# Performance work log

Measured on AMD Instinct MI355X. Metric: run time of the kernel, lower is better.

The kernel has to match this reference:

```python
import jax, jax.numpy as jnp
import numpy as np

N_NODES = 50000
N_EDGES = 800000
IN_CH, HIDDEN, OUT_CH = 64, 16, 8


def setup_inputs() -> dict:
    key = jax.random.key(0)
    ks = jax.random.split(key, 8)
    x = jax.random.normal(ks[0], (N_NODES, IN_CH), dtype=jnp.float32)
    edge_index = jax.random.randint(ks[1], (2, N_EDGES), 0, N_NODES, dtype=jnp.int64)
    # SAGEConv params: lin_l (neighbor aggregate, has bias), lin_r (root, no bias)
    s1 = 1.0 / np.sqrt(IN_CH)
    s2 = 1.0 / np.sqrt(HIDDEN)
    W1l = jax.random.uniform(ks[2], (HIDDEN, IN_CH), jnp.float32, -s1, s1)
    W1r = jax.random.uniform(ks[3], (HIDDEN, IN_CH), jnp.float32, -s1, s1)
    b1 = jax.random.uniform(ks[4], (HIDDEN,), jnp.float32, -s1, s1)
    W2l = jax.random.uniform(ks[5], (OUT_CH, HIDDEN), jnp.float32, -s2, s2)
    W2r = jax.random.uniform(ks[6], (OUT_CH, HIDDEN), jnp.float32, -s2, s2)
    b2 = jax.random.uniform(ks[7], (OUT_CH,), jnp.float32, -s2, s2)
    return {"x": x, "W1l": W1l, "W1r": W1r, "b1": b1,
            "W2l": W2l, "W2r": W2r, "b2": b2, "edge_index": edge_index}


def _sage_conv(x, src, dst, Wl, Wr, b, n_nodes):
    # mean-aggregate neighbor features: gather from src, scatter-mean to dst
    msg_sum = jax.ops.segment_sum(x[src], dst, num_segments=n_nodes)  # [N, d]
    deg = jax.ops.segment_sum(jnp.ones((src.shape[0], 1), x.dtype), dst,
                              num_segments=n_nodes)                    # [N, 1]
    aggr = msg_sum / jnp.maximum(deg, 1.0)
    # out = lin_l(aggr) + lin_r(x); bias lives in lin_l
    return aggr @ Wl.T + x @ Wr.T + b


def reference(x, W1l, W1r, b1, W2l, W2r, b2, edge_index):
    src, dst = edge_index[0], edge_index[1]
    n = x.shape[0]
    h = jax.nn.relu(_sage_conv(x, src, dst, W1l, W1r, b1, n))
    # F.dropout(p=0.1, training=self.training): identity in eval mode
    return _sage_conv(h, src, dst, W2l, W2r, b2, n)
```

## Files before the change

kernel.cpp:

```cpp
#include <hip/hip_runtime.h>

#define IN_CH 64
#define HID   16
#define OUTC  8
#define BINSHIFT 6
#define BINCAP  (1 << BINSHIFT)

#define CHUNK_A     1024
#define SLICE_SHIFT 8
#define SLICE_NODES 256
#define SUBCAP      24

typedef _Float16 half2_t __attribute__((ext_vector_type(2)));
typedef _Float16 half8_t __attribute__((ext_vector_type(8)));


__global__ __launch_bounds__(256) void build_xform(
    const float* __restrict__ x,
    const int*   __restrict__ esrc,
    const int*   __restrict__ edst,
    const float* __restrict__ W1l,
    const float* __restrict__ W1r,
    const float* __restrict__ b1,
    int* __restrict__ cnts,
    unsigned int* __restrict__ gbuf,
    _Float16* __restrict__ y1h,
    float* __restrict__ r1,
    int n_nodes, int n_edges, int nb_part)
{
    __shared__ __align__(16) float sWl[HID * 68];
    __shared__ __align__(16) float sWr[HID * 68];
    __shared__ __align__(16) float sx[16 * 68];
    __shared__ float sb1[HID];
    __shared__ int scurs[SLICE_NODES];

    int b   = blockIdx.x;
    int tid = threadIdx.x;

    if (b < nb_part) {
        int base = b * CHUNK_A;
        scurs[tid] = 0;
        __syncthreads();
#pragma unroll
        for (int j = 0; j < CHUNK_A / 256; ++j) {
            int e = base + j * 256 + tid;
            if (e < n_edges) {
                int d  = edst[e];
                int s  = esrc[e];
                int bk = d >> SLICE_SHIFT;
                int pos = atomicAdd(&scurs[bk], 1);
                if (pos < SUBCAP)
                    gbuf[((size_t)bk * nb_part + b) * SUBCAP + pos] =
                        (unsigned)(s & 0xFFFF) |
                        ((unsigned)(d & (SLICE_NODES - 1)) << 16);
            }
        }
        __syncthreads();
        int c = scurs[tid];
        cnts[(size_t)tid * nb_part + b] = c > SUBCAP ? SUBCAP : c;
        return;
    }

    for (int i = tid; i < HID * IN_CH; i += 256) {
        int c = i >> 6, k = i & 63;
        sWl[c * 68 + k] = W1l[i];
        sWr[c * 68 + k] = W1r[i];
    }
    if (tid < HID) sb1[tid] = b1[tid];

    int nl   = tid >> 4;
    int c    = tid & 15;
    int node = (b - nb_part) * 16 + nl;

    if (node < n_nodes)
        *(float4*)&sx[nl * 68 + c * 4] =
            *(const float4*)&x[(size_t)node * IN_CH + c * 4];
    __syncthreads();
    if (node >= n_nodes) return;

    float accL = 0.f, accR = 0.f;
#pragma unroll
    for (int k4 = 0; k4 < 16; ++k4) {
        float4 xv = *(const float4*)&sx [nl * 68 + k4 * 4];
        float4 wl = *(const float4*)&sWl[c  * 68 + k4 * 4];
        float4 wr = *(const float4*)&sWr[c  * 68 + k4 * 4];
        accL = fmaf(xv.x, wl.x, accL); accL = fmaf(xv.y, wl.y, accL);
        accL = fmaf(xv.z, wl.z, accL); accL = fmaf(xv.w, wl.w, accL);
        accR = fmaf(xv.x, wr.x, accR); accR = fmaf(xv.y, wr.y, accR);
        accR = fmaf(xv.z, wr.z, accR); accR = fmaf(xv.w, wr.w, accR);
    }
    y1h[(size_t)node * HID + c] = (_Float16)accL;
    r1 [(size_t)node * HID + c] = accR + sb1[c];
}

__global__ __launch_bounds__(256) void bin_build(
    const int* __restrict__ cnts,
    const unsigned int* __restrict__ gbuf,
    int* __restrict__ cur,
    unsigned short* __restrict__ adj,
    int n_nodes, int nb_part)
{
    __shared__ int scnt[SLICE_NODES];
    __shared__ __align__(16) unsigned short bins[SLICE_NODES * BINCAP];

    int b   = blockIdx.x;
    int tid = threadIdx.x;

    scnt[tid] = 0;
    __syncthreads();

    for (int a = tid; a < nb_part; a += 256) {
        int cnt = cnts[(size_t)b * nb_part + a];
        const unsigned int* bp = gbuf + ((size_t)b * nb_part + a) * SUBCAP;
        for (int i = 0; i < cnt; ++i) {
            unsigned p = bp[i];
            int dl  = p >> 16;
            int pos = atomicAdd(&scnt[dl], 1);
            if (pos < BINCAP)
                bins[(dl << BINSHIFT) + pos] = (unsigned short)(p & 0xFFFF);
        }
    }
    __syncthreads();

    int node0  = b << SLICE_SHIFT;
    int nvalid = n_nodes - node0;
    if (nvalid > SLICE_NODES) nvalid = SLICE_NODES;

    if (tid < nvalid) cur[node0 + tid] = scnt[tid];

    int nv = nvalid << 3;
    for (int i = tid; i < nv; i += 256)
        *(uint4*)(adj + ((size_t)node0 << BINSHIFT) + ((size_t)i << 3)) =
            *(const uint4*)&bins[(size_t)i << 3];
}

#define ACC8(v)                                                          \
    do {                                                                 \
        half2_t p01 = {(v).s0, (v).s1}, p23 = {(v).s2, (v).s3};          \
        half2_t p45 = {(v).s4, (v).s5}, p67 = {(v).s6, (v).s7};          \
        s0 = __builtin_amdgcn_fdot2(p01, k10, s0, false);                \
        s1 = __builtin_amdgcn_fdot2(p01, k01, s1, false);                \
        s2 = __builtin_amdgcn_fdot2(p23, k10, s2, false);                \
        s3 = __builtin_amdgcn_fdot2(p23, k01, s3, false);                \
        s4 = __builtin_amdgcn_fdot2(p45, k10, s4, false);                \
        s5 = __builtin_amdgcn_fdot2(p45, k01, s5, false);                \
        s6 = __builtin_amdgcn_fdot2(p67, k10, s6, false);                \
        s7 = __builtin_amdgcn_fdot2(p67, k01, s7, false);                \
    } while (0)

__global__ __launch_bounds__(256) void fused_gather(
    const float* __restrict__ r1,
    const _Float16* __restrict__ y1h,
    const int*   __restrict__ cur,
    const unsigned short* __restrict__ adj,
    const float* __restrict__ W2l, const float* __restrict__ W2r,
    const float* __restrict__ b2,
    _Float16* __restrict__ y2h, float* __restrict__ r2out,
    int n_nodes)
{
    __shared__ float sW2l[HID * OUTC];
    __shared__ float sW2r[HID * OUTC];
    __shared__ float sb2[OUTC];
    __shared__ float sh[32 * 17];

    int tid = threadIdx.x;
    for (int i = tid; i < HID * OUTC; i += 256) {
        int o = i >> 4, k = i & 15;
        sW2l[k * OUTC + o] = W2l[i];
        sW2r[k * OUTC + o] = W2r[i];
    }
    if (tid < OUTC) sb2[tid] = b2[tid];

    int nl   = tid >> 3;
    int t    = tid & 7;
    int h    = t >> 2;
    int ep   = t & 3;
    int node = blockIdx.x * 32 + nl;
    bool real = node < n_nodes;

    const half2_t k10 = {(_Float16)1.f, (_Float16)0.f};
    const half2_t k01 = {(_Float16)0.f, (_Float16)1.f};

    if (real) {
        int deg = cur[node];
        if (deg > BINCAP) deg = BINCAP;
        int iters = deg >> 2;
        float s0 = 0.f, s1 = 0.f, s2 = 0.f, s3 = 0.f;
        float s4 = 0.f, s5 = 0.f, s6 = 0.f, s7 = 0.f;
        const _Float16* yq = y1h + h * 8;
        const unsigned short* row = adj + ((size_t)node << BINSHIFT);
        const ushort4* ap = (const ushort4*)row;
        for (int it = ep; it < iters; it += 4) {
            ushort4 s = ap[it];
            half8_t v0 = *(const half8_t*)(yq + (size_t)s.x * HID);
            half8_t v1 = *(const half8_t*)(yq + (size_t)s.y * HID);
            half8_t v2 = *(const half8_t*)(yq + (size_t)s.z * HID);
            half8_t v3 = *(const half8_t*)(yq + (size_t)s.w * HID);
            ACC8(v0); ACC8(v1); ACC8(v2); ACC8(v3);
        }
        for (int g = (iters << 2) + ep; g < deg; g += 4) {
            half8_t v = *(const half8_t*)(yq + (size_t)row[g] * HID);
            ACC8(v);
        }
        s0 += __shfl_xor(s0, 1); s0 += __shfl_xor(s0, 2);
        s1 += __shfl_xor(s1, 1); s1 += __shfl_xor(s1, 2);
        s2 += __shfl_xor(s2, 1); s2 += __shfl_xor(s2, 2);
        s3 += __shfl_xor(s3, 1); s3 += __shfl_xor(s3, 2);
        s4 += __shfl_xor(s4, 1); s4 += __shfl_xor(s4, 2);
        s5 += __shfl_xor(s5, 1); s5 += __shfl_xor(s5, 2);
        s6 += __shfl_xor(s6, 1); s6 += __shfl_xor(s6, 2);
        s7 += __shfl_xor(s7, 1); s7 += __shfl_xor(s7, 2);

        if (ep == 0) {
            float inv = 1.0f / fmaxf((float)deg, 1.0f);
            const float* rr = &r1[(size_t)node * HID + h * 8];
            float4 ra = *(const float4*)(rr);
            float4 rb = *(const float4*)(rr + 4);
            float* shp = &sh[nl * 17 + h * 8];
            shp[0] = fmaxf(fmaf(s0, inv, ra.x), 0.f);
            shp[1] = fmaxf(fmaf(s1, inv, ra.y), 0.f);
            shp[2] = fmaxf(fmaf(s2, inv, ra.z), 0.f);
            shp[3] = fmaxf(fmaf(s3, inv, ra.w), 0.f);
            shp[4] = fmaxf(fmaf(s4, inv, rb.x), 0.f);
            shp[5] = fmaxf(fmaf(s5, inv, rb.y), 0.f);
            shp[6] = fmaxf(fmaf(s6, inv, rb.z), 0.f);
            shp[7] = fmaxf(fmaf(s7, inv, rb.w), 0.f);
        }
    }
    __syncthreads();
    if (!real) return;

    const float* hrow = &sh[nl * 17];
    float al = 0.f, ar = sb2[t];
#pragma unroll
    for (int k = 0; k < HID; ++k) {
        float hv = hrow[k];
        al = fmaf(hv, sW2l[k * OUTC + t], al);
        ar = fmaf(hv, sW2r[k * OUTC + t], ar);
    }
    y2h[(size_t)node * OUTC + t] = (_Float16)al;
    r2out[(size_t)node * OUTC + t] = ar;
}

__global__ __launch_bounds__(256) void gather_out(
    const _Float16* __restrict__ y2h,
    const int*   __restrict__ cur,
    const unsigned short* __restrict__ adj,
    float* __restrict__ out,
    int n_nodes)
{
    int tid  = threadIdx.x;
    int node = blockIdx.x * 64 + (tid >> 2);
    if (node >= n_nodes) return;
    int ep = tid & 3;

    int deg = cur[node];
    if (deg > BINCAP) deg = BINCAP;
    int iters = deg >> 2;
    const unsigned short* row = adj + ((size_t)node << BINSHIFT);
    const ushort4* ap = (const ushort4*)row;

    const half2_t k10 = {(_Float16)1.f, (_Float16)0.f};
    const half2_t k01 = {(_Float16)0.f, (_Float16)1.f};

    float s0 = 0.f, s1 = 0.f, s2 = 0.f, s3 = 0.f;
    float s4 = 0.f, s5 = 0.f, s6 = 0.f, s7 = 0.f;
    for (int it = ep; it < iters; it += 4) {
        ushort4 s = ap[it];
        half8_t v0 = *(const half8_t*)(y2h + (size_t)s.x * OUTC);
        half8_t v1 = *(const half8_t*)(y2h + (size_t)s.y * OUTC);
        half8_t v2 = *(const half8_t*)(y2h + (size_t)s.z * OUTC);
        half8_t v3 = *(const half8_t*)(y2h + (size_t)s.w * OUTC);
        ACC8(v0); ACC8(v1); ACC8(v2); ACC8(v3);
    }
    for (int g = (iters << 2) + ep; g < deg; g += 4) {
        half8_t v = *(const half8_t*)(y2h + (size_t)row[g] * OUTC);
        ACC8(v);
    }
    s0 += __shfl_xor(s0, 1); s0 += __shfl_xor(s0, 2);
    s1 += __shfl_xor(s1, 1); s1 += __shfl_xor(s1, 2);
    s2 += __shfl_xor(s2, 1); s2 += __shfl_xor(s2, 2);
    s3 += __shfl_xor(s3, 1); s3 += __shfl_xor(s3, 2);
    s4 += __shfl_xor(s4, 1); s4 += __shfl_xor(s4, 2);
    s5 += __shfl_xor(s5, 1); s5 += __shfl_xor(s5, 2);
    s6 += __shfl_xor(s6, 1); s6 += __shfl_xor(s6, 2);
    s7 += __shfl_xor(s7, 1); s7 += __shfl_xor(s7, 2);
    if (ep != 0) return;

    float inv = 1.0f / fmaxf((float)deg, 1.0f);
    float* op = out + (size_t)node * OUTC;
    float4 c0 = *(float4*)op;
    float4 c1 = *(float4*)(op + 4);
    c0.x = fmaf(s0, inv, c0.x); c0.y = fmaf(s1, inv, c0.y);
    c0.z = fmaf(s2, inv, c0.z); c0.w = fmaf(s3, inv, c0.w);
    c1.x = fmaf(s4, inv, c1.x); c1.y = fmaf(s5, inv, c1.y);
    c1.z = fmaf(s6, inv, c1.z); c1.w = fmaf(s7, inv, c1.w);
    *(float4*)op = c0;
    *(float4*)(op + 4) = c1;
}

extern "C" void kernel_launch(void* const* d_in, const int* in_sizes, int n_in,
                              void* d_out, int out_size, void* d_ws, size_t ws_size,
                              hipStream_t stream)
{
    const float* x   = (const float*)d_in[0];
    const float* W1l = (const float*)d_in[1];
    const float* W1r = (const float*)d_in[2];
    const float* b1  = (const float*)d_in[3];
    const float* W2l = (const float*)d_in[4];
    const float* W2r = (const float*)d_in[5];
    const float* b2  = (const float*)d_in[6];
    const int*   ei  = (const int*)d_in[7];

    int n_nodes = in_sizes[0] / IN_CH;
    int n_edges = in_sizes[7] / 2;
    const int* esrc = ei;
    const int* edst = ei + n_edges;

    float* out = (float*)d_out;

    dim3 blk(256);
    int nb_part = (n_edges + CHUNK_A - 1) / CHUNK_A;
    int nb_node = (n_nodes + 15) / 16;
    int ns      = (n_nodes + SLICE_NODES - 1) >> SLICE_SHIFT;

    char* wsb = (char*)d_ws;
    _Float16* y1h = (_Float16*)wsb;
    _Float16* y2h = y1h + (size_t)n_nodes * HID;
    float* r1 = (float*)(y2h + (size_t)n_nodes * OUTC);
    int* cur  = (int*)(r1 + (size_t)n_nodes * HID);
    unsigned short* adj = (unsigned short*)(cur + n_nodes);
    int* cnts = (int*)(adj + ((size_t)n_nodes << BINSHIFT));
    unsigned int* gbuf = (unsigned int*)(cnts + (size_t)SLICE_NODES * nb_part);

    build_xform<<<dim3(nb_part + nb_node), blk, 0, stream>>>(
        x, esrc, edst, W1l, W1r, b1, cnts, gbuf, y1h, r1,
        n_nodes, n_edges, nb_part);

    bin_build<<<dim3(ns), blk, 0, stream>>>(cnts, gbuf, cur, adj,
                                            n_nodes, nb_part);

    fused_gather<<<dim3((n_nodes + 31) / 32), blk, 0, stream>>>(
        r1, y1h, cur, adj, W2l, W2r, b2, y2h, out, n_nodes);

    gather_out<<<dim3((n_nodes + 63) / 64), blk, 0, stream>>>(
        y2h, cur, adj, out, n_nodes);
}
```

Measured before the change: 119.4 us.

## Merge four kernels into one cooperative persistent kernel with grid syncs

Replaces the four separate launches (edge partition plus layer-1 transform, bin build, fused layer-1 gather plus layer-2 transform, output gather) with a single cooperative kernel of fixed grid size that loops over virtual blocks and separates phases with grid.sync. The aim is to remove per-launch overhead and inter-kernel gaps. In exchange, the grid is capped at 1024 blocks with shared memory reused across phases, and each grid-wide barrier makes every block wait for the slowest one. The phase-2 split gives bin building a fixed set of blocks while the rest do the transform, so occupancy and load balance change.

```diff
diff --git a/kernel.cpp b/kernel.cpp
--- a/kernel.cpp
+++ b/kernel.cpp
@@ -1,4 +1,7 @@
 #include <hip/hip_runtime.h>
+#include <hip/hip_cooperative_groups.h>
+
+namespace cg = cooperative_groups;
 
 #define IN_CH 64
 #define HID   16
@@ -11,128 +14,12 @@
 #define SLICE_NODES 256
 #define SUBCAP      24
 
+#define NBLOCKS     1024
+#define SMEM_BYTES  33792
+
 typedef _Float16 half2_t __attribute__((ext_vector_type(2)));
 typedef _Float16 half8_t __attribute__((ext_vector_type(8)));
 
-
-__global__ __launch_bounds__(256) void build_xform(
-    const float* __restrict__ x,
-    const int*   __restrict__ esrc,
-    const int*   __restrict__ edst,
-    const float* __restrict__ W1l,
-    const float* __restrict__ W1r,
-    const float* __restrict__ b1,
-    int* __restrict__ cnts,
-    unsigned int* __restrict__ gbuf,
-    _Float16* __restrict__ y1h,
-    float* __restrict__ r1,
-    int n_nodes, int n_edges, int nb_part)
-{
-    __shared__ __align__(16) float sWl[HID * 68];
-    __shared__ __align__(16) float sWr[HID * 68];
-    __shared__ __align__(16) float sx[16 * 68];
-    __shared__ float sb1[HID];
-    __shared__ int scurs[SLICE_NODES];
-
-    int b   = blockIdx.x;
-    int tid = threadIdx.x;
-
-    if (b < nb_part) {
-        int base = b * CHUNK_A;
-        scurs[tid] = 0;
-        __syncthreads();
-#pragma unroll
-        for (int j = 0; j < CHUNK_A / 256; ++j) {
-            int e = base + j * 256 + tid;
-            if (e < n_edges) {
-                int d  = edst[e];
-                int s  = esrc[e];
-                int bk = d >> SLICE_SHIFT;
-                int pos = atomicAdd(&scurs[bk], 1);
-                if (pos < SUBCAP)
-                    gbuf[((size_t)bk * nb_part + b) * SUBCAP + pos] =
-                        (unsigned)(s & 0xFFFF) |
-                        ((unsigned)(d & (SLICE_NODES - 1)) << 16);
-            }
-        }
-        __syncthreads();
-        int c = scurs[tid];
-        cnts[(size_t)tid * nb_part + b] = c > SUBCAP ? SUBCAP : c;
-        return;
-    }
-
-    for (int i = tid; i < HID * IN_CH; i += 256) {
-        int c = i >> 6, k = i & 63;
-        sWl[c * 68 + k] = W1l[i];
-        sWr[c * 68 + k] = W1r[i];
-    }
-    if (tid < HID) sb1[tid] = b1[tid];
-
-    int nl   = tid >> 4;
-    int c    = tid & 15;
-    int node = (b - nb_part) * 16 + nl;
-
-    if (node < n_nodes)
-        *(float4*)&sx[nl * 68 + c * 4] =
-            *(const float4*)&x[(size_t)node * IN_CH + c * 4];
-    __syncthreads();
-    if (node >= n_nodes) return;
-
-    float accL = 0.f, accR = 0.f;
-#pragma unroll
-    for (int k4 = 0; k4 < 16; ++k4) {
-        float4 xv = *(const float4*)&sx [nl * 68 + k4 * 4];
-        float4 wl = *(const float4*)&sWl[c  * 68 + k4 * 4];
-        float4 wr = *(const float4*)&sWr[c  * 68 + k4 * 4];
-        accL = fmaf(xv.x, wl.x, accL); accL = fmaf(xv.y, wl.y, accL);
-        accL = fmaf(xv.z, wl.z, accL); accL = fmaf(xv.w, wl.w, accL);
-        accR = fmaf(xv.x, wr.x, accR); accR = fmaf(xv.y, wr.y, accR);
-        accR = fmaf(xv.z, wr.z, accR); accR = fmaf(xv.w, wr.w, accR);
-    }
-    y1h[(size_t)node * HID + c] = (_Float16)accL;
-    r1 [(size_t)node * HID + c] = accR + sb1[c];
-}
-
-__global__ __launch_bounds__(256) void bin_build(
-    const int* __restrict__ cnts,
-    const unsigned int* __restrict__ gbuf,
-    int* __restrict__ cur,
-    unsigned short* __restrict__ adj,
-    int n_nodes, int nb_part)
-{
-    __shared__ int scnt[SLICE_NODES];
-    __shared__ __align__(16) unsigned short bins[SLICE_NODES * BINCAP];
-
-    int b   = blockIdx.x;
-    int tid = threadIdx.x;
-
-    scnt[tid] = 0;
-    __syncthreads();
-
-    for (int a = tid; a < nb_part; a += 256) {
-        int cnt = cnts[(size_t)b * nb_part + a];
-        const unsigned int* bp = gbuf + ((size_t)b * nb_part + a) * SUBCAP;
-        for (int i = 0; i < cnt; ++i) {
-            unsigned p = bp[i];
-            int dl  = p >> 16;
-            int pos = atomicAdd(&scnt[dl], 1);
-            if (pos < BINCAP)
-                bins[(dl << BINSHIFT) + pos] = (unsigned short)(p & 0xFFFF);
-        }
-    }
-    __syncthreads();
-
-    int node0  = b << SLICE_SHIFT;
-    int nvalid = n_nodes - node0;
-    if (nvalid > SLICE_NODES) nvalid = SLICE_NODES;
-
-    if (tid < nvalid) cur[node0 + tid] = scnt[tid];
-
-    int nv = nvalid << 3;
-    for (int i = tid; i < nv; i += 256)
-        *(uint4*)(adj + ((size_t)node0 << BINSHIFT) + ((size_t)i << 3)) =
-            *(const uint4*)&bins[(size_t)i << 3];
-}
 
 #define ACC8(v)                                                          \
     do {                                                                 \
@@ -148,155 +35,257 @@
         s7 = __builtin_amdgcn_fdot2(p67, k01, s7, false);                \
     } while (0)
 
-__global__ __launch_bounds__(256) void fused_gather(
-    const float* __restrict__ r1,
-    const _Float16* __restrict__ y1h,
-    const int*   __restrict__ cur,
-    const unsigned short* __restrict__ adj,
-    const float* __restrict__ W2l, const float* __restrict__ W2r,
+__global__ __launch_bounds__(256, 4) void sage_all(
+    const float* __restrict__ x,
+    const int*   __restrict__ esrc,
+    const int*   __restrict__ edst,
+    const float* __restrict__ W1l,
+    const float* __restrict__ W1r,
+    const float* __restrict__ b1,
+    const float* __restrict__ W2l,
+    const float* __restrict__ W2r,
     const float* __restrict__ b2,
-    _Float16* __restrict__ y2h, float* __restrict__ r2out,
-    int n_nodes)
+    int* __restrict__ cnts,
+    unsigned int* __restrict__ gbuf,
+    _Float16* __restrict__ y1h,
+    float* __restrict__ r1,
+    int* __restrict__ cur,
+    unsigned short* __restrict__ adj,
+    _Float16* __restrict__ y2h,
+    float* __restrict__ out,
+    int n_nodes, int n_edges, int nb_part, int nb_node, int ns)
 {
-    __shared__ float sW2l[HID * OUTC];
-    __shared__ float sW2r[HID * OUTC];
-    __shared__ float sb2[OUTC];
-    __shared__ float sh[32 * 17];
-
-    int tid = threadIdx.x;
-    for (int i = tid; i < HID * OUTC; i += 256) {
-        int o = i >> 4, k = i & 15;
-        sW2l[k * OUTC + o] = W2l[i];
-        sW2r[k * OUTC + o] = W2r[i];
-    }
-    if (tid < OUTC) sb2[tid] = b2[tid];
-
-    int nl   = tid >> 3;
-    int t    = tid & 7;
-    int h    = t >> 2;
-    int ep   = t & 3;
-    int node = blockIdx.x * 32 + nl;
-    bool real = node < n_nodes;
+    cg::grid_group grid = cg::this_grid();
+    __shared__ __align__(16) char smem[SMEM_BYTES];
+    const int tid = threadIdx.x;
+    const int bid = blockIdx.x;
+    const int gsz = gridDim.x;
 
     const half2_t k10 = {(_Float16)1.f, (_Float16)0.f};
     const half2_t k01 = {(_Float16)0.f, (_Float16)1.f};
 
-    if (real) {
-        int deg = cur[node];
-        if (deg > BINCAP) deg = BINCAP;
-        int iters = deg >> 2;
-        float s0 = 0.f, s1 = 0.f, s2 = 0.f, s3 = 0.f;
-        float s4 = 0.f, s5 = 0.f, s6 = 0.f, s7 = 0.f;
-        const _Float16* yq = y1h + h * 8;
-        const unsigned short* row = adj + ((size_t)node << BINSHIFT);
-        const ushort4* ap = (const ushort4*)row;
-        for (int it = ep; it < iters; it += 4) {
-            ushort4 s = ap[it];
-            half8_t v0 = *(const half8_t*)(yq + (size_t)s.x * HID);
-            half8_t v1 = *(const half8_t*)(yq + (size_t)s.y * HID);
-            half8_t v2 = *(const half8_t*)(yq + (size_t)s.z * HID);
-            half8_t v3 = *(const half8_t*)(yq + (size_t)s.w * HID);
-            ACC8(v0); ACC8(v1); ACC8(v2); ACC8(v3);
-        }
-        for (int g = (iters << 2) + ep; g < deg; g += 4) {
-            half8_t v = *(const half8_t*)(yq + (size_t)row[g] * HID);
-            ACC8(v);
-        }
-        s0 += __shfl_xor(s0, 1); s0 += __shfl_xor(s0, 2);
-        s1 += __shfl_xor(s1, 1); s1 += __shfl_xor(s1, 2);
-        s2 += __shfl_xor(s2, 1); s2 += __shfl_xor(s2, 2);
-        s3 += __shfl_xor(s3, 1); s3 += __shfl_xor(s3, 2);
-        s4 += __shfl_xor(s4, 1); s4 += __shfl_xor(s4, 2);
-        s5 += __shfl_xor(s5, 1); s5 += __shfl_xor(s5, 2);
-        s6 += __shfl_xor(s6, 1); s6 += __shfl_xor(s6, 2);
-        s7 += __shfl_xor(s7, 1); s7 += __shfl_xor(s7, 2);
-
-        if (ep == 0) {
+    {
+        int* scurs = (int*)smem;
+        for (int vb = bid; vb < nb_part; vb += gsz) {
+            scurs[tid] = 0;
+            __syncthreads();
+            int base = vb * CHUNK_A;
+#pragma unroll
+            for (int j = 0; j < CHUNK_A / 256; ++j) {
+                int e = base + j * 256 + tid;
+                if (e < n_edges) {
+                    int d  = edst[e];
+                    int s  = esrc[e];
+                    int bk = d >> SLICE_SHIFT;
+                    int pos = atomicAdd(&scurs[bk], 1);
+                    if (pos < SUBCAP)
+                        gbuf[((size_t)bk * nb_part + vb) * SUBCAP + pos] =
+                            (unsigned)(s & 0xFFFF) |
+                            ((unsigned)(d & (SLICE_NODES - 1)) << 16);
+                }
+            }
+            __syncthreads();
+            int c = scurs[tid];
+            cnts[(size_t)tid * nb_part + vb] = c > SUBCAP ? SUBCAP : c;
+            __syncthreads();
+        }
+    }
+    grid.sync();
+
+    if (bid < ns) {
+        int* scnt = (int*)smem;
+        unsigned short* bins = (unsigned short*)(smem + 1024);
+        int b = bid;
+        scnt[tid] = 0;
+        __syncthreads();
+        for (int a = tid; a < nb_part; a += 256) {
+            int cnt = cnts[(size_t)b * nb_part + a];
+            const unsigned int* bp = gbuf + ((size_t)b * nb_part + a) * SUBCAP;
+            for (int i = 0; i < cnt; ++i) {
+                unsigned p = bp[i];
+                int dl  = p >> 16;
+                int pos = atomicAdd(&scnt[dl], 1);
+                if (pos < BINCAP)
+                    bins[(dl << BINSHIFT) + pos] = (unsigned short)(p & 0xFFFF);
+            }
+        }
+        __syncthreads();
+        int node0  = b << SLICE_SHIFT;
+        int nvalid = n_nodes - node0;
+        if (nvalid > SLICE_NODES) nvalid = SLICE_NODES;
+        if (tid < nvalid) cur[node0 + tid] = scnt[tid];
+        int nv = nvalid << 3;
+        for (int i = tid; i < nv; i += 256)
+            *(uint4*)(adj + ((size_t)node0 << BINSHIFT) + ((size_t)i << 3)) =
+                *(const uint4*)&bins[(size_t)i << 3];
+    } else {
+        float* sWl = (float*)smem;
+        float* sWr = (float*)(smem + 4352);
+        float* sx  = (float*)(smem + 8704);
+        float* sb1 = (float*)(smem + 13056);
+        for (int i = tid; i < HID * IN_CH; i += 256) {
+            int c = i >> 6, k = i & 63;
+            sWl[c * 68 + k] = W1l[i];
+            sWr[c * 68 + k] = W1r[i];
+        }
+        if (tid < HID) sb1[tid] = b1[tid];
+        int nl = tid >> 4;
+        int c  = tid & 15;
+        for (int vb = bid - ns; vb < nb_node; vb += gsz - ns) {
+            __syncthreads();
+            int node = vb * 16 + nl;
+            if (node < n_nodes)
+                *(float4*)&sx[nl * 68 + c * 4] =
+                    *(const float4*)&x[(size_t)node * IN_CH + c * 4];
+            __syncthreads();
+            if (node < n_nodes) {
+                float accL = 0.f, accR = 0.f;
+#pragma unroll
+                for (int k4 = 0; k4 < 16; ++k4) {
+                    float4 xv = *(const float4*)&sx [nl * 68 + k4 * 4];
+                    float4 wl = *(const float4*)&sWl[c  * 68 + k4 * 4];
+                    float4 wr = *(const float4*)&sWr[c  * 68 + k4 * 4];
+                    accL = fmaf(xv.x, wl.x, accL); accL = fmaf(xv.y, wl.y, accL);
+                    accL = fmaf(xv.z, wl.z, accL); accL = fmaf(xv.w, wl.w, accL);
+                    accR = fmaf(xv.x, wr.x, accR); accR = fmaf(xv.y, wr.y, accR);
+                    accR = fmaf(xv.z, wr.z, accR); accR = fmaf(xv.w, wr.w, accR);
+                }
+                y1h[(size_t)node * HID + c] = (_Float16)accL;
+                r1 [(size_t)node * HID + c] = accR + sb1[c];
+            }
+        }
+    }
+    grid.sync();
+
+    {
+        float* sW2l = (float*)smem;
+        float* sW2r = (float*)(smem + 512);
+        float* sb2  = (float*)(smem + 1024);
+        float* sh   = (float*)(smem + 1088);
+        for (int i = tid; i < HID * OUTC; i += 256) {
+            int o = i >> 4, k = i & 15;
+            sW2l[k * OUTC + o] = W2l[i];
+            sW2r[k * OUTC + o] = W2r[i];
+        }
+        if (tid < OUTC) sb2[tid] = b2[tid];
+
+        int nl = tid >> 3;
+        int t  = tid & 7;
+        int h  = t >> 2;
+        int ep = t & 3;
+        int nb_g2 = (n_nodes + 31) >> 5;
+        for (int vb = bid; vb < nb_g2; vb += gsz) {
+            __syncthreads();
+            int node = vb * 32 + nl;
+            bool real = node < n_nodes;
+            if (real) {
+                int deg = cur[node];
+                if (deg > BINCAP) deg = BINCAP;
+                int iters = deg >> 2;
+                float s0 = 0.f, s1 = 0.f, s2 = 0.f, s3 = 0.f;
+                float s4 = 0.f, s5 = 0.f, s6 = 0.f, s7 = 0.f;
+                const _Float16* yq = y1h + h * 8;
+                const unsigned short* row = adj + ((size_t)node << BINSHIFT);
+                const ushort4* ap = (const ushort4*)row;
+                for (int it = ep; it < iters; it += 4) {
+                    ushort4 s = ap[it];
+                    half8_t v0 = *(const half8_t*)(yq + (size_t)s.x * HID);
+                    half8_t v1 = *(const half8_t*)(yq + (size_t)s.y * HID);
+                    half8_t v2 = *(const half8_t*)(yq + (size_t)s.z * HID);
+                    half8_t v3 = *(const half8_t*)(yq + (size_t)s.w * HID);
+                    ACC8(v0); ACC8(v1); ACC8(v2); ACC8(v3);
+                }
+                for (int g = (iters << 2) + ep; g < deg; g += 4) {
+                    half8_t v = *(const half8_t*)(yq + (size_t)row[g] * HID);
+                    ACC8(v);
+                }
+                s0 += __shfl_xor(s0, 1); s0 += __shfl_xor(s0, 2);
+                s1 += __shfl_xor(s1, 1); s1 += __shfl_xor(s1, 2);
+                s2 += __shfl_xor(s2, 1); s2 += __shfl_xor(s2, 2);
+                s3 += __shfl_xor(s3, 1); s3 += __shfl_xor(s3, 2);
+                s4 += __shfl_xor(s4, 1); s4 += __shfl_xor(s4, 2);
+                s5 += __shfl_xor(s5, 1); s5 += __shfl_xor(s5, 2);
+                s6 += __shfl_xor(s6, 1); s6 += __shfl_xor(s6, 2);
+                s7 += __shfl_xor(s7, 1); s7 += __shfl_xor(s7, 2);
+                if (ep == 0) {
+                    float inv = 1.0f / fmaxf((float)deg, 1.0f);
+                    const float* rr = &r1[(size_t)node * HID + h * 8];
+                    float4 ra = *(const float4*)(rr);
+                    float4 rb = *(const float4*)(rr + 4);
+                    float* shp = &sh[nl * 17 + h * 8];
+                    shp[0] = fmaxf(fmaf(s0, inv, ra.x), 0.f);
+                    shp[1] = fmaxf(fmaf(s1, inv, ra.y), 0.f);
+                    shp[2] = fmaxf(fmaf(s2, inv, ra.z), 0.f);
+                    shp[3] = fmaxf(fmaf(s3, inv, ra.w), 0.f);
+                    shp[4] = fmaxf(fmaf(s4, inv, rb.x), 0.f);
+                    shp[5] = fmaxf(fmaf(s5, inv, rb.y), 0.f);
+                    shp[6] = fmaxf(fmaf(s6, inv, rb.z), 0.f);
+                    shp[7] = fmaxf(fmaf(s7, inv, rb.w), 0.f);
+                }
+            }
+            __syncthreads();
+            if (real) {
+                const float* hrow = &sh[nl * 17];
+                float al = 0.f, ar = sb2[t];
+#pragma unroll
+                for (int k = 0; k < HID; ++k) {
+                    float hv = hrow[k];
+                    al = fmaf(hv, sW2l[k * OUTC + t], al);
+                    ar = fmaf(hv, sW2r[k * OUTC + t], ar);
+                }
+                y2h[(size_t)node * OUTC + t] = (_Float16)al;
+                out[(size_t)node * OUTC + t] = ar;
+            }
+        }
+    }
+    grid.sync();
+
+    {
+        int nb_g3 = (n_nodes + 63) >> 6;
+        for (int vb = bid; vb < nb_g3; vb += gsz) {
+            int node = vb * 64 + (tid >> 2);
+            if (node >= n_nodes) continue;
+            int ep = tid & 3;
+            int deg = cur[node];
+            if (deg > BINCAP) deg = BINCAP;
+            int iters = deg >> 2;
+            const unsigned short* row = adj + ((size_t)node << BINSHIFT);
+            const ushort4* ap = (const ushort4*)row;
+            float s0 = 0.f, s1 = 0.f, s2 = 0.f, s3 = 0.f;
+            float s4 = 0.f, s5 = 0.f, s6 = 0.f, s7 = 0.f;
+            for (int it = ep; it < iters; it += 4) {
+                ushort4 s = ap[it];
+                half8_t v0 = *(const half8_t*)(y2h + (size_t)s.x * OUTC);
+                half8_t v1 = *(const half8_t*)(y2h + (size_t)s.y * OUTC);
+                half8_t v2 = *(const half8_t*)(y2h + (size_t)s.z * OUTC);
+                half8_t v3 = *(const half8_t*)(y2h + (size_t)s.w * OUTC);
+                ACC8(v0); ACC8(v1); ACC8(v2); ACC8(v3);
+            }
+            for (int g = (iters << 2) + ep; g < deg; g += 4) {
+                half8_t v = *(const half8_t*)(y2h + (size_t)row[g] * OUTC);
+                ACC8(v);
+            }
+            s0 += __shfl_xor(s0, 1); s0 += __shfl_xor(s0, 2);
+            s1 += __shfl_xor(s1, 1); s1 += __shfl_xor(s1, 2);
+            s2 += __shfl_xor(s2, 1); s2 += __shfl_xor(s2, 2);
+            s3 += __shfl_xor(s3, 1); s3 += __shfl_xor(s3, 2);
+            s4 += __shfl_xor(s4, 1); s4 += __shfl_xor(s4, 2);
+            s5 += __shfl_xor(s5, 1); s5 += __shfl_xor(s5, 2);
+            s6 += __shfl_xor(s6, 1); s6 += __shfl_xor(s6, 2);
+            s7 += __shfl_xor(s7, 1); s7 += __shfl_xor(s7, 2);
+            if (ep != 0) continue;
             float inv = 1.0f / fmaxf((float)deg, 1.0f);
-            const float* rr = &r1[(size_t)node * HID + h * 8];
-            float4 ra = *(const float4*)(rr);
-            float4 rb = *(const float4*)(rr + 4);
-            float* shp = &sh[nl * 17 + h * 8];
-            shp[0] = fmaxf(fmaf(s0, inv, ra.x), 0.f);
-            shp[1] = fmaxf(fmaf(s1, inv, ra.y), 0.f);
-            shp[2] = fmaxf(fmaf(s2, inv, ra.z), 0.f);
-            shp[3] = fmaxf(fmaf(s3, inv, ra.w), 0.f);
-            shp[4] = fmaxf(fmaf(s4, inv, rb.x), 0.f);
-            shp[5] = fmaxf(fmaf(s5, inv, rb.y), 0.f);
-            shp[6] = fmaxf(fmaf(s6, inv, rb.z), 0.f);
-            shp[7] = fmaxf(fmaf(s7, inv, rb.w), 0.f);
+            float* op = out + (size_t)node * OUTC;
+            float4 c0 = *(float4*)op;
+            float4 c1 = *(float4*)(op + 4);
+            c0.x = fmaf(s0, inv, c0.x); c0.y = fmaf(s1, inv, c0.y);
+            c0.z = fmaf(s2, inv, c0.z); c0.w = fmaf(s3, inv, c0.w);
+            c1.x = fmaf(s4, inv, c1.x); c1.y = fmaf(s5, inv, c1.y);
+            c1.z = fmaf(s6, inv, c1.z); c1.w = fmaf(s7, inv, c1.w);
+            *(float4*)op = c0;
+            *(float4*)(op + 4) = c1;
         }
     }
-    __syncthreads();
-    if (!real) return;
-
-    const float* hrow = &sh[nl * 17];
-    float al = 0.f, ar = sb2[t];
-#pragma unroll
-    for (int k = 0; k < HID; ++k) {
-        float hv = hrow[k];
-        al = fmaf(hv, sW2l[k * OUTC + t], al);
-        ar = fmaf(hv, sW2r[k * OUTC + t], ar);
-    }
-    y2h[(size_t)node * OUTC + t] = (_Float16)al;
-    r2out[(size_t)node * OUTC + t] = ar;
-}
-
-__global__ __launch_bounds__(256) void gather_out(
-    const _Float16* __restrict__ y2h,
-    const int*   __restrict__ cur,
-    const unsigned short* __restrict__ adj,
-    float* __restrict__ out,
-    int n_nodes)
-{
-    int tid  = threadIdx.x;
-    int node = blockIdx.x * 64 + (tid >> 2);
-    if (node >= n_nodes) return;
-    int ep = tid & 3;
-
-    int deg = cur[node];
-    if (deg > BINCAP) deg = BINCAP;
-    int iters = deg >> 2;
-    const unsigned short* row = adj + ((size_t)node << BINSHIFT);
-    const ushort4* ap = (const ushort4*)row;
-
-    const half2_t k10 = {(_Float16)1.f, (_Float16)0.f};
-    const half2_t k01 = {(_Float16)0.f, (_Float16)1.f};
-
-    float s0 = 0.f, s1 = 0.f, s2 = 0.f, s3 = 0.f;
-    float s4 = 0.f, s5 = 0.f, s6 = 0.f, s7 = 0.f;
-    for (int it = ep; it < iters; it += 4) {
-        ushort4 s = ap[it];
-        half8_t v0 = *(const half8_t*)(y2h + (size_t)s.x * OUTC);
-        half8_t v1 = *(const half8_t*)(y2h + (size_t)s.y * OUTC);
-        half8_t v2 = *(const half8_t*)(y2h + (size_t)s.z * OUTC);
-        half8_t v3 = *(const half8_t*)(y2h + (size_t)s.w * OUTC);
-        ACC8(v0); ACC8(v1); ACC8(v2); ACC8(v3);
-    }
-    for (int g = (iters << 2) + ep; g < deg; g += 4) {
-        half8_t v = *(const half8_t*)(y2h + (size_t)row[g] * OUTC);
-        ACC8(v);
-    }
-    s0 += __shfl_xor(s0, 1); s0 += __shfl_xor(s0, 2);
-    s1 += __shfl_xor(s1, 1); s1 += __shfl_xor(s1, 2);
-    s2 += __shfl_xor(s2, 1); s2 += __shfl_xor(s2, 2);
-    s3 += __shfl_xor(s3, 1); s3 += __shfl_xor(s3, 2);
-    s4 += __shfl_xor(s4, 1); s4 += __shfl_xor(s4, 2);
-    s5 += __shfl_xor(s5, 1); s5 += __shfl_xor(s5, 2);
-    s6 += __shfl_xor(s6, 1); s6 += __shfl_xor(s6, 2);
-    s7 += __shfl_xor(s7, 1); s7 += __shfl_xor(s7, 2);
-    if (ep != 0) return;
-
-    float inv = 1.0f / fmaxf((float)deg, 1.0f);
-    float* op = out + (size_t)node * OUTC;
-    float4 c0 = *(float4*)op;
-    float4 c1 = *(float4*)(op + 4);
-    c0.x = fmaf(s0, inv, c0.x); c0.y = fmaf(s1, inv, c0.y);
-    c0.z = fmaf(s2, inv, c0.z); c0.w = fmaf(s3, inv, c0.w);
-    c1.x = fmaf(s4, inv, c1.x); c1.y = fmaf(s5, inv, c1.y);
-    c1.z = fmaf(s6, inv, c1.z); c1.w = fmaf(s7, inv, c1.w);
-    *(float4*)op = c0;
-    *(float4*)(op + 4) = c1;
 }
 
 extern "C" void kernel_launch(void* const* d_in, const int* in_sizes, int n_in,
@@ -319,7 +308,6 @@
 
     float* out = (float*)d_out;
 
-    dim3 blk(256);
     int nb_part = (n_edges + CHUNK_A - 1) / CHUNK_A;
     int nb_node = (n_nodes + 15) / 16;
     int ns      = (n_nodes + SLICE_NODES - 1) >> SLICE_SHIFT;
@@ -333,16 +321,15 @@
     int* cnts = (int*)(adj + ((size_t)n_nodes << BINSHIFT));
     unsigned int* gbuf = (unsigned int*)(cnts + (size_t)SLICE_NODES * nb_part);
 
-    build_xform<<<dim3(nb_part + nb_node), blk, 0, stream>>>(
-        x, esrc, edst, W1l, W1r, b1, cnts, gbuf, y1h, r1,
-        n_nodes, n_edges, nb_part);
-
-    bin_build<<<dim3(ns), blk, 0, stream>>>(cnts, gbuf, cur, adj,
-                                            n_nodes, nb_part);
-
-    fused_gather<<<dim3((n_nodes + 31) / 32), blk, 0, stream>>>(
-        r1, y1h, cur, adj, W2l, W2r, b2, y2h, out, n_nodes);
-
-    gather_out<<<dim3((n_nodes + 63) / 64), blk, 0, stream>>>(
-        y2h, cur, adj, out, n_nodes);
+    void* args[] = {
+        (void*)&x, (void*)&esrc, (void*)&edst,
+        (void*)&W1l, (void*)&W1r, (void*)&b1,
+        (void*)&W2l, (void*)&W2r, (void*)&b2,
+        (void*)&cnts, (void*)&gbuf, (void*)&y1h, (void*)&r1,
+        (void*)&cur, (void*)&adj, (void*)&y2h, (void*)&out,
+        (void*)&n_nodes, (void*)&n_edges, (void*)&nb_part,
+        (void*)&nb_node, (void*)&ns };
+
+    hipLaunchCooperativeKernel((void*)sage_all, dim3(NBLOCKS), dim3(256),
+                               args, 0, stream);
 }
```

After: 474.7 us. 297% more time.

## Fuse adjacency bin build into layer-1 gather and inline partition counts

Applied to the files above, without the earlier changes.

Removes the separate bin_build kernel: each slice block now builds its per-node neighbor bins in shared memory and immediately runs the layer-1 gather and layer-2 transform from those shared bins, while still writing cur/adj for the final gather. Slices shrink to 128 nodes, and per-partition counts are stored as the first word of each 16-word gbuf record instead of a separate cnts array. This saves a kernel launch and a global round-trip of the adjacency list. In exchange, per-partition capacity drops to 15 edges per slice, which risks dropping edges when a partition exceeds it. Grid parallelism also falls to about 391 blocks, each doing serial batches.

```diff
diff --git a/kernel.cpp b/kernel.cpp
--- a/kernel.cpp
+++ b/kernel.cpp
@@ -7,9 +7,10 @@
 #define BINCAP  (1 << BINSHIFT)
 
 #define CHUNK_A     1024
-#define SLICE_SHIFT 8
-#define SLICE_NODES 256
-#define SUBCAP      24
+#define SLICE_SHIFT 7
+#define SLICE_NODES 128
+#define NSL_PAD     392
+#define SUBWORDS    16
 
 typedef _Float16 half2_t __attribute__((ext_vector_type(2)));
 typedef _Float16 half8_t __attribute__((ext_vector_type(8)));
@@ -22,25 +23,24 @@
     const float* __restrict__ W1l,
     const float* __restrict__ W1r,
     const float* __restrict__ b1,
-    int* __restrict__ cnts,
     unsigned int* __restrict__ gbuf,
     _Float16* __restrict__ y1h,
     float* __restrict__ r1,
-    int n_nodes, int n_edges, int nb_part)
+    int n_nodes, int n_edges, int nb_part, int nsl)
 {
     __shared__ __align__(16) float sWl[HID * 68];
     __shared__ __align__(16) float sWr[HID * 68];
     __shared__ __align__(16) float sx[16 * 68];
     __shared__ float sb1[HID];
-    __shared__ int scurs[SLICE_NODES];
+    __shared__ int scurs[NSL_PAD];
 
     int b   = blockIdx.x;
     int tid = threadIdx.x;
 
     if (b < nb_part) {
+        for (int i = tid; i < nsl; i += 256) scurs[i] = 0;
+        __syncthreads();
         int base = b * CHUNK_A;
-        scurs[tid] = 0;
-        __syncthreads();
 #pragma unroll
         for (int j = 0; j < CHUNK_A / 256; ++j) {
             int e = base + j * 256 + tid;
@@ -49,15 +49,18 @@
                 int s  = esrc[e];
                 int bk = d >> SLICE_SHIFT;
                 int pos = atomicAdd(&scurs[bk], 1);
-                if (pos < SUBCAP)
-                    gbuf[((size_t)bk * nb_part + b) * SUBCAP + pos] =
-                        (unsigned)(s & 0xFFFF) |
+                if (pos < SUBWORDS - 1)
+                    gbuf[((size_t)bk * nb_part + b) * SUBWORDS + 1 + pos] =
+                        (unsigned)s |
                         ((unsigned)(d & (SLICE_NODES - 1)) << 16);
             }
         }
         __syncthreads();
-        int c = scurs[tid];
-        cnts[(size_t)tid * nb_part + b] = c > SUBCAP ? SUBCAP : c;
+        for (int i = tid; i < nsl; i += 256) {
+            int c = scurs[i];
+            gbuf[((size_t)i * nb_part + b) * SUBWORDS] =
+                c > SUBWORDS - 1 ? SUBWORDS - 1 : c;
+        }
         return;
     }
 
@@ -91,47 +94,6 @@
     }
     y1h[(size_t)node * HID + c] = (_Float16)accL;
     r1 [(size_t)node * HID + c] = accR + sb1[c];
-}
-
-__global__ __launch_bounds__(256) void bin_build(
-    const int* __restrict__ cnts,
-    const unsigned int* __restrict__ gbuf,
-    int* __restrict__ cur,
-    unsigned short* __restrict__ adj,
-    int n_nodes, int nb_part)
-{
-    __shared__ int scnt[SLICE_NODES];
-    __shared__ __align__(16) unsigned short bins[SLICE_NODES * BINCAP];
-
-    int b   = blockIdx.x;
-    int tid = threadIdx.x;
-
-    scnt[tid] = 0;
-    __syncthreads();
-
-    for (int a = tid; a < nb_part; a += 256) {
-        int cnt = cnts[(size_t)b * nb_part + a];
-        const unsigned int* bp = gbuf + ((size_t)b * nb_part + a) * SUBCAP;
-        for (int i = 0; i < cnt; ++i) {
-            unsigned p = bp[i];
-            int dl  = p >> 16;
-            int pos = atomicAdd(&scnt[dl], 1);
-            if (pos < BINCAP)
-                bins[(dl << BINSHIFT) + pos] = (unsigned short)(p & 0xFFFF);
-        }
-    }
-    __syncthreads();
-
-    int node0  = b << SLICE_SHIFT;
-    int nvalid = n_nodes - node0;
-    if (nvalid > SLICE_NODES) nvalid = SLICE_NODES;
-
-    if (tid < nvalid) cur[node0 + tid] = scnt[tid];
-
-    int nv = nvalid << 3;
-    for (int i = tid; i < nv; i += 256)
-        *(uint4*)(adj + ((size_t)node0 << BINSHIFT) + ((size_t)i << 3)) =
-            *(const uint4*)&bins[(size_t)i << 3];
 }
 
 #define ACC8(v)                                                          \
@@ -148,98 +110,130 @@
         s7 = __builtin_amdgcn_fdot2(p67, k01, s7, false);                \
     } while (0)
 
-__global__ __launch_bounds__(256) void fused_gather(
+__global__ __launch_bounds__(256) void slice_gather(
     const float* __restrict__ r1,
     const _Float16* __restrict__ y1h,
-    const int*   __restrict__ cur,
-    const unsigned short* __restrict__ adj,
+    const unsigned int* __restrict__ gbuf,
     const float* __restrict__ W2l, const float* __restrict__ W2r,
     const float* __restrict__ b2,
-    _Float16* __restrict__ y2h, float* __restrict__ r2out,
-    int n_nodes)
+    int* __restrict__ cur,
+    unsigned short* __restrict__ adj,
+    _Float16* __restrict__ y2h, float* __restrict__ out,
+    int n_nodes, int nb_part)
 {
+    __shared__ int scnt[SLICE_NODES];
+    __shared__ __align__(16) unsigned short bins[SLICE_NODES * BINCAP];
     __shared__ float sW2l[HID * OUTC];
     __shared__ float sW2r[HID * OUTC];
     __shared__ float sb2[OUTC];
     __shared__ float sh[32 * 17];
 
+    int b   = blockIdx.x;
     int tid = threadIdx.x;
+
     for (int i = tid; i < HID * OUTC; i += 256) {
         int o = i >> 4, k = i & 15;
         sW2l[k * OUTC + o] = W2l[i];
         sW2r[k * OUTC + o] = W2r[i];
     }
     if (tid < OUTC) sb2[tid] = b2[tid];
-
-    int nl   = tid >> 3;
-    int t    = tid & 7;
-    int h    = t >> 2;
-    int ep   = t & 3;
-    int node = blockIdx.x * 32 + nl;
-    bool real = node < n_nodes;
+    if (tid < SLICE_NODES) scnt[tid] = 0;
+    __syncthreads();
+
+    for (int a = tid; a < nb_part; a += 256) {
+        const unsigned int* bp = gbuf + ((size_t)b * nb_part + a) * SUBWORDS;
+        int cnt = (int)bp[0];
+        for (int i = 0; i < cnt; ++i) {
+            unsigned p = bp[1 + i];
+            int dl  = p >> 16;
+            int pos = atomicAdd(&scnt[dl], 1);
+            if (pos < BINCAP)
+                bins[(dl << BINSHIFT) + pos] = (unsigned short)p;
+        }
+    }
+    __syncthreads();
+
+    int node0  = b << SLICE_SHIFT;
+    int nvalid = n_nodes - node0;
+    if (nvalid > SLICE_NODES) nvalid = SLICE_NODES;
+
+    if (tid < nvalid) cur[node0 + tid] = scnt[tid];
+    int nv = nvalid << 3;
+    for (int i = tid; i < nv; i += 256)
+        *(uint4*)(adj + ((size_t)node0 << BINSHIFT) + ((size_t)i << 3)) =
+            *(const uint4*)&bins[(size_t)i << 3];
+
+    int nl = tid >> 3;
+    int t  = tid & 7;
+    int h  = t >> 2;
+    int ep = t & 3;
 
     const half2_t k10 = {(_Float16)1.f, (_Float16)0.f};
     const half2_t k01 = {(_Float16)0.f, (_Float16)1.f};
 
-    if (real) {
-        int deg = cur[node];
-        if (deg > BINCAP) deg = BINCAP;
-        int iters = deg >> 2;
-        float s0 = 0.f, s1 = 0.f, s2 = 0.f, s3 = 0.f;
-        float s4 = 0.f, s5 = 0.f, s6 = 0.f, s7 = 0.f;
-        const _Float16* yq = y1h + h * 8;
-        const unsigned short* row = adj + ((size_t)node << BINSHIFT);
-        const ushort4* ap = (const ushort4*)row;
-        for (int it = ep; it < iters; it += 4) {
-            ushort4 s = ap[it];
-            half8_t v0 = *(const half8_t*)(yq + (size_t)s.x * HID);
-            half8_t v1 = *(const half8_t*)(yq + (size_t)s.y * HID);
-            half8_t v2 = *(const half8_t*)(yq + (size_t)s.z * HID);
-            half8_t v3 = *(const half8_t*)(yq + (size_t)s.w * HID);
-            ACC8(v0); ACC8(v1); ACC8(v2); ACC8(v3);
-        }
-        for (int g = (iters << 2) + ep; g < deg; g += 4) {
-            half8_t v = *(const half8_t*)(yq + (size_t)row[g] * HID);
-            ACC8(v);
-        }
-        s0 += __shfl_xor(s0, 1); s0 += __shfl_xor(s0, 2);
-        s1 += __shfl_xor(s1, 1); s1 += __shfl_xor(s1, 2);
-        s2 += __shfl_xor(s2, 1); s2 += __shfl_xor(s2, 2);
-        s3 += __shfl_xor(s3, 1); s3 += __shfl_xor(s3, 2);
-        s4 += __shfl_xor(s4, 1); s4 += __shfl_xor(s4, 2);
-        s5 += __shfl_xor(s5, 1); s5 += __shfl_xor(s5, 2);
-        s6 += __shfl_xor(s6, 1); s6 += __shfl_xor(s6, 2);
-        s7 += __shfl_xor(s7, 1); s7 += __shfl_xor(s7, 2);
-
-        if (ep == 0) {
-            float inv = 1.0f / fmaxf((float)deg, 1.0f);
-            const float* rr = &r1[(size_t)node * HID + h * 8];
-            float4 ra = *(const float4*)(rr);
-            float4 rb = *(const float4*)(rr + 4);
-            float* shp = &sh[nl * 17 + h * 8];
-            shp[0] = fmaxf(fmaf(s0, inv, ra.x), 0.f);
-            shp[1] = fmaxf(fmaf(s1, inv, ra.y), 0.f);
-            shp[2] = fmaxf(fmaf(s2, inv, ra.z), 0.f);
-            shp[3] = fmaxf(fmaf(s3, inv, ra.w), 0.f);
-            shp[4] = fmaxf(fmaf(s4, inv, rb.x), 0.f);
-            shp[5] = fmaxf(fmaf(s5, inv, rb.y), 0.f);
-            shp[6] = fmaxf(fmaf(s6, inv, rb.z), 0.f);
-            shp[7] = fmaxf(fmaf(s7, inv, rb.w), 0.f);
-        }
-    }
-    __syncthreads();
-    if (!real) return;
-
-    const float* hrow = &sh[nl * 17];
-    float al = 0.f, ar = sb2[t];
+    for (int batch = 0; batch < SLICE_NODES / 32; ++batch) {
+        __syncthreads();
+        int ln   = batch * 32 + nl;
+        int node = node0 + ln;
+        bool real = ln < nvalid;
+        if (real) {
+            int deg = scnt[ln];
+            if (deg > BINCAP) deg = BINCAP;
+            int iters = deg >> 2;
+            float s0 = 0.f, s1 = 0.f, s2 = 0.f, s3 = 0.f;
+            float s4 = 0.f, s5 = 0.f, s6 = 0.f, s7 = 0.f;
+            const _Float16* yq = y1h + h * 8;
+            const unsigned short* row = &bins[ln << BINSHIFT];
+            for (int it = ep; it < iters; it += 4) {
+                ushort4 s = *(const ushort4*)(row + (it << 2));
+                half8_t v0 = *(const half8_t*)(yq + (size_t)s.x * HID);
+                half8_t v1 = *(const half8_t*)(yq + (size_t)s.y * HID);
+                half8_t v2 = *(const half8_t*)(yq + (size_t)s.z * HID);
+                half8_t v3 = *(const half8_t*)(yq + (size_t)s.w * HID);
+                ACC8(v0); ACC8(v1); ACC8(v2); ACC8(v3);
+            }
+            for (int g = (iters << 2) + ep; g < deg; g += 4) {
+                half8_t v = *(const half8_t*)(yq + (size_t)row[g] * HID);
+                ACC8(v);
+            }
+            s0 += __shfl_xor(s0, 1); s0 += __shfl_xor(s0, 2);
+            s1 += __shfl_xor(s1, 1); s1 += __shfl_xor(s1, 2);
+            s2 += __shfl_xor(s2, 1); s2 += __shfl_xor(s2, 2);
+            s3 += __shfl_xor(s3, 1); s3 += __shfl_xor(s3, 2);
+            s4 += __shfl_xor(s4, 1); s4 += __shfl_xor(s4, 2);
+            s5 += __shfl_xor(s5, 1); s5 += __shfl_xor(s5, 2);
+            s6 += __shfl_xor(s6, 1); s6 += __shfl_xor(s6, 2);
+            s7 += __shfl_xor(s7, 1); s7 += __shfl_xor(s7, 2);
+            if (ep == 0) {
+                float inv = 1.0f / fmaxf((float)deg, 1.0f);
+                const float* rr = &r1[(size_t)node * HID + h * 8];
+                float4 ra = *(const float4*)(rr);
+                float4 rb = *(const float4*)(rr + 4);
+                float* shp = &sh[nl * 17 + h * 8];
+                shp[0] = fmaxf(fmaf(s0, inv, ra.x), 0.f);
+                shp[1] = fmaxf(fmaf(s1, inv, ra.y), 0.f);
+                shp[2] = fmaxf(fmaf(s2, inv, ra.z), 0.f);
+                shp[3] = fmaxf(fmaf(s3, inv, ra.w), 0.f);
+                shp[4] = fmaxf(fmaf(s4, inv, rb.x), 0.f);
+                shp[5] = fmaxf(fmaf(s5, inv, rb.y), 0.f);
+                shp[6] = fmaxf(fmaf(s6, inv, rb.z), 0.f);
+                shp[7] = fmaxf(fmaf(s7, inv, rb.w), 0.f);
+            }
+        }
+        __syncthreads();
+        if (real) {
+            const float* hrow = &sh[nl * 17];
+            float al = 0.f, ar = sb2[t];
 #pragma unroll
-    for (int k = 0; k < HID; ++k) {
-        float hv = hrow[k];
-        al = fmaf(hv, sW2l[k * OUTC + t], al);
-        ar = fmaf(hv, sW2r[k * OUTC + t], ar);
-    }
-    y2h[(size_t)node * OUTC + t] = (_Float16)al;
-    r2out[(size_t)node * OUTC + t] = ar;
+            for (int k = 0; k < HID; ++k) {
+                float hv = hrow[k];
+                al = fmaf(hv, sW2l[k * OUTC + t], al);
+                ar = fmaf(hv, sW2r[k * OUTC + t], ar);
+            }
+            y2h[(size_t)node * OUTC + t] = (_Float16)al;
+            out[(size_t)node * OUTC + t] = ar;
+        }
+    }
 }
 
 __global__ __launch_bounds__(256) void gather_out(
@@ -319,10 +313,9 @@
 
     float* out = (float*)d_out;
 
-    dim3 blk(256);
     int nb_part = (n_edges + CHUNK_A - 1) / CHUNK_A;
     int nb_node = (n_nodes + 15) / 16;
-    int ns      = (n_nodes + SLICE_NODES - 1) >> SLICE_SHIFT;
+    int nsl     = (n_nodes + SLICE_NODES - 1) >> SLICE_SHIFT;
 
     char* wsb = (char*)d_ws;
     _Float16* y1h = (_Float16*)wsb;
@@ -330,18 +323,17 @@
     float* r1 = (float*)(y2h + (size_t)n_nodes * OUTC);
     int* cur  = (int*)(r1 + (size_t)n_nodes * HID);
     unsigned short* adj = (unsigned short*)(cur + n_nodes);
-    int* cnts = (int*)(adj + ((size_t)n_nodes << BINSHIFT));
-    unsigned int* gbuf = (unsigned int*)(cnts + (size_t)SLICE_NODES * nb_part);
+    unsigned int* gbuf = (unsigned int*)(adj + ((size_t)n_nodes << BINSHIFT));
+
+    dim3 blk(256);
 
     build_xform<<<dim3(nb_part + nb_node), blk, 0, stream>>>(
-        x, esrc, edst, W1l, W1r, b1, cnts, gbuf, y1h, r1,
-        n_nodes, n_edges, nb_part);
-
-    bin_build<<<dim3(ns), blk, 0, stream>>>(cnts, gbuf, cur, adj,
-                                            n_nodes, nb_part);
-
-    fused_gather<<<dim3((n_nodes + 31) / 32), blk, 0, stream>>>(
-        r1, y1h, cur, adj, W2l, W2r, b2, y2h, out, n_nodes);
+        x, esrc, edst, W1l, W1r, b1, gbuf, y1h, r1,
+        n_nodes, n_edges, nb_part, nsl);
+
+    slice_gather<<<dim3(nsl), blk, 0, stream>>>(
+        r1, y1h, gbuf, W2l, W2r, b2, cur, adj, y2h, out,
+        n_nodes, nb_part);
 
     gather_out<<<dim3((n_nodes + 63) / 64), blk, 0, stream>>>(
         y2h, cur, adj, out, n_nodes);
```

Result: no change. 118.9 us (-0.5%).
